# Kernel optimization log

Measured on AMD Instinct MI355X. Metric: run time of the kernel, lower is better.

## Reference

```python
import jax, jax.numpy as jnp
import numpy as np

B, N_X, N_A, DIM = 2, 2048, 2048, 1024
HEADS, DH = 16, 64
SEG = 256
ROPE_THETA = 10000.0


def mh_rmsnorm(t, gamma):
    # t: [b,h,n,d], gamma: [h,1,d]; F.normalize(dim=-1) * gamma * sqrt(d)
    norm = jnp.linalg.norm(t, axis=-1, keepdims=True)
    return t / jnp.clip(norm, 1e-12) * gamma * (DH ** 0.5)


def apply_rope(t):
    # t: [b,h,n,d]; GPT-NeoX style half-split rotary over packed positions
    n = t.shape[2]
    half = DH // 2
    inv_freq = ROPE_THETA ** (-jnp.arange(0, half, dtype=jnp.float32) / half)
    freqs = jnp.arange(n, dtype=jnp.float32)[:, None] * inv_freq[None, :]  # [n, half]
    cos, sin = jnp.cos(freqs), jnp.sin(freqs)
    t1, t2 = t[..., :half], t[..., half:]
    return jnp.concatenate([t1 * cos - t2 * sin, t2 * cos + t1 * sin], axis=-1)


def infini_attention(q, k, v, beta):
    # q,k,v: [b,h,n,d]; causal local attention per segment + recurrent linear memory
    b, h, n, d = q.shape
    s = n // SEG
    scale = d ** -0.5
    gate = jax.nn.sigmoid(beta).reshape(1, h, 1, 1)
    causal = jnp.tril(jnp.ones((SEG, SEG), dtype=bool))

    def to_segs(t):  # -> [s, b, h, SEG, d]
        return jnp.moveaxis(t.reshape(b, h, s, SEG, d), 2, 0)

    qs, ks, vs = to_segs(q), to_segs(k), to_segs(v)

    def step(carry, inp):
        M, z = carry  # M: [b,h,d,d], z: [b,h,d]
        q_s, k_s, v_s = inp
        sq = jax.nn.elu(q_s) + 1.0
        sk = jax.nn.elu(k_s) + 1.0
        # memory retrieval
        num = jnp.einsum('bhld,bhde->bhle', sq, M)
        den = jnp.einsum('bhld,bhd->bhl', sq, z)[..., None] + 1e-6
        a_mem = num / den
        # local causal attention within segment
        scores = jnp.einsum('bhid,bhjd->bhij', q_s, k_s) * scale
        scores = jnp.where(causal, scores, -jnp.inf)
        a_loc = jnp.einsum('bhij,bhjd->bhid', jax.nn.softmax(scores, axis=-1), v_s)
        out = gate * a_mem + (1.0 - gate) * a_loc
        # memory update
        M = M + jnp.einsum('bhld,bhle->bhde', sk, v_s)
        z = z + sk.sum(axis=2)
        return (M, z), out

    M0 = jnp.zeros((b, h, d, d), dtype=q.dtype)
    z0 = jnp.zeros((b, h, d), dtype=q.dtype)
    _, outs = jax.lax.scan(step, (M0, z0), (qs, ks, vs))  # [s,b,h,SEG,d]
    return jnp.moveaxis(outs, 0, 2).reshape(b, h, n, d)


def setup_inputs() -> dict:
    key = jax.random.key(0)
    ks = jax.random.split(key, 4)
    scale = DIM ** -0.5
    x = jax.random.normal(ks[0], (B, N_X, DIM), dtype=jnp.float32)
    a = jax.random.normal(ks[1], (B, N_A, DIM), dtype=jnp.float32)
    w_qkv_x = jax.random.normal(ks[2], (DIM, 3 * HEADS * DH), dtype=jnp.float32) * scale
    w_qkv_a = jax.random.normal(ks[3], (DIM, 3 * HEADS * DH), dtype=jnp.float32) * scale
    g = lambda: jnp.ones((HEADS, 1, DH), dtype=jnp.float32)
    beta = jnp.zeros((HEADS,), dtype=jnp.float32)
    return {"x": x, "a": a, "w_qkv_x": w_qkv_x, "w_qkv_a": w_qkv_a,
            "gq_x": g(), "gk_x": g(), "gq_a": g(), "gk_a": g(), "beta": beta}


def _split_heads(t):
    b, n, _ = t.shape
    q, k, v = jnp.split(t, 3, axis=-1)
    r = lambda u: u.reshape(b, n, HEADS, DH).transpose(0, 2, 1, 3)
    return r(q), r(k), r(v)


def reference(x, a, w_qkv_x, w_qkv_a, gq_x, gk_x, gq_a, gk_a, beta):
    q_x, k_x, v_x = _split_heads(x @ w_qkv_x)
    q_a, k_a, v_a = _split_heads(a @ w_qkv_a)
    q_x, k_x = mh_rmsnorm(q_x, gq_x), mh_rmsnorm(k_x, gk_x)
    q_a, k_a = mh_rmsnorm(q_a, gq_a), mh_rmsnorm(k_a, gk_a)
    # pack: a-stream first, then x-stream (matches pack([._a, ._x]))
    q = jnp.concatenate([q_a, q_x], axis=2)
    k = jnp.concatenate([k_a, k_x], axis=2)
    v = jnp.concatenate([v_a, v_x], axis=2)
    q, k = apply_rope(q), apply_rope(k)
    out = infini_attention(q, k, v, beta)  # [b,h,n_a+n_x,d]
    out_a, out_x = out[:, :, :N_A], out[:, :, N_A:]
    merge = lambda t: t.transpose(0, 2, 1, 3).reshape(t.shape[0], t.shape[2], HEADS * DH)
    return merge(out_x), merge(out_a)
```

## Files before the change

kernel.cpp:

```cpp
#include <hip/hip_runtime.h>

#define HEADS 16
#define DH    64
#define NA    2048
#define NX    2048
#define NTOT  4096
#define DIMK  1024
#define NQKV  3072
#define SEG   256
#define NSEG  16

typedef float          f32x4  __attribute__((ext_vector_type(4)));
typedef short          bf16x8 __attribute__((ext_vector_type(8)));
typedef unsigned int   u32x4  __attribute__((ext_vector_type(4)));

__device__ __forceinline__ unsigned short f2bf(float f){
  unsigned int u = __builtin_bit_cast(unsigned int, f);
  unsigned int r = 0x7fffu + ((u >> 16) & 1u);
  return (unsigned short)((u + r) >> 16);
}
__device__ __forceinline__ float bf2f(unsigned short u){
  return __builtin_bit_cast(float, ((unsigned int)u) << 16);
}

__global__ __launch_bounds__(256) void zero_kernel(float* __restrict__ out, int n){
  int i = blockIdx.x * 256 + threadIdx.x;
  if (i < n) out[i] = 0.f;
}

__global__ __launch_bounds__(256) void cvt_kernel(const float* __restrict__ src,
                                                  unsigned short* __restrict__ dst, int n4){
  int i = blockIdx.x * 256 + threadIdx.x;
  if (i >= n4) return;
  float4 v = ((const float4*)src)[i];
  ushort4 o;
  o.x = f2bf(v.x); o.y = f2bf(v.y); o.z = f2bf(v.z); o.w = f2bf(v.w);
  ((ushort4*)dst)[i] = o;
}

__global__ __launch_bounds__(256) void wtr_kernel(const float* __restrict__ W,
                                                  unsigned short* __restrict__ WT){
  __shared__ float tile[32][33];
  int c0 = blockIdx.x * 32, k0 = blockIdx.y * 32;
  int tx = threadIdx.x, ty = threadIdx.y;
  #pragma unroll
  for (int i = 0; i < 32; i += 8) tile[ty+i][tx] = W[(size_t)(k0+ty+i)*NQKV + c0 + tx];
  __syncthreads();
  #pragma unroll
  for (int i = 0; i < 32; i += 8) WT[(size_t)(c0+ty+i)*DIMK + k0 + tx] = f2bf(tile[tx][ty+i]);
}

__global__ __launch_bounds__(256) void rope_tab_kernel(float* __restrict__ tab){
  const int idx = blockIdx.x * 256 + threadIdx.x;
  const int n = idx >> 5, d = idx & 31;
  const float ang = (float)n * expf(-(float)d * 0.28782313662425572f);
  float sn, cs;
  sincosf(ang, &sn, &cs);
  float2 p; p.x = cs; p.y = sn;
  ((float2*)tab)[idx] = p;
}

__global__ __launch_bounds__(256,2) void gemm_qkv_kernel(
    const unsigned short* __restrict__ Xb, const unsigned short* __restrict__ Ab,
    const unsigned short* __restrict__ WTx, const unsigned short* __restrict__ WTa,
    unsigned short* __restrict__ qb, unsigned short* __restrict__ kb,
    unsigned short* __restrict__ vt,
    const float* __restrict__ gqx, const float* __restrict__ gkx,
    const float* __restrict__ gqa, const float* __restrict__ gka,
    const float* __restrict__ tab)
{
  __shared__ __align__(16) unsigned short As[128*32];
  __shared__ __align__(16) unsigned short Bs[128*32];
  const int strm = blockIdx.z;
  const unsigned short* Xp = strm ? Ab  : Xb;
  const unsigned short* Wp = strm ? WTa : WTx;
  const float* gq = strm ? gqa : gqx;
  const float* gk = strm ? gka : gkx;
  const int n_off = strm ? 0 : NA;

  const int tid  = threadIdx.x;
  const int lane = tid & 63, w = tid >> 6;
  const int wr = w >> 1, wc = w & 1;
  const int li = lane & 15, lg = lane >> 4;
  const int m0 = blockIdx.y * 128, c0 = blockIdx.x * 128;

  const int srow = lane >> 2;
  const int sslot = lane & 3;
  const int sswz = sslot ^ (srow & 3) ^ ((srow >> 2) & 3);
  const int rswz = (li & 3) ^ ((li >> 2) & 3);

  f32x4 acc[4][4] = {};

  for (int k0 = 0; k0 < DIMK; k0 += 32){
    __syncthreads();
    #pragma unroll
    for (int jj = 0; jj < 2; jj++){
      const int j = 2*w + jj;
      const int r = j*16 + srow;
      __builtin_amdgcn_global_load_lds(
        (const __attribute__((address_space(1))) unsigned int*)(Xp + (size_t)(m0+r)*DIMK + k0 + sswz*8),
        (__attribute__((address_space(3))) unsigned int*)(As + j*512), 16, 0, 0);
      __builtin_amdgcn_global_load_lds(
        (const __attribute__((address_space(1))) unsigned int*)(Wp + (size_t)(c0+r)*DIMK + k0 + sswz*8),
        (__attribute__((address_space(3))) unsigned int*)(Bs + j*512), 16, 0, 0);
    }
    __syncthreads();
    bf16x8 af[4], bf[4];
    const int slot = (lg ^ rswz) * 8;
    #pragma unroll
    for (int m = 0; m < 4; m++){
      const int r = wr*64 + m*16 + li;
      af[m] = *(const bf16x8*)(&As[r*32 + slot]);
    }
    #pragma unroll
    for (int n = 0; n < 4; n++){
      const int r = wc*64 + n*16 + li;
      bf[n] = *(const bf16x8*)(&Bs[r*32 + slot]);
    }
    #pragma unroll
    for (int m = 0; m < 4; m++)
      #pragma unroll
      for (int n = 0; n < 4; n++)
        acc[m][n] = __builtin_amdgcn_mfma_f32_16x16x32_bf16(af[m], bf[n], acc[m][n], 0, 0, 0);
  }

  const int colbase = c0 + wc*64;
  const int which = colbase >> 10;
  const int h = (colbase >> 6) & 15;

  if (which < 2){
    const float* gv = (which == 0) ? gq : gk;
    unsigned short* dstb = (which == 0) ? qb : kb;
    float gl[4];
    #pragma unroll
    for (int n = 0; n < 4; n++) gl[n] = gv[h*64 + n*16 + li];
    #pragma unroll
    for (int m = 0; m < 4; m++){
      #pragma unroll
      for (int r = 0; r < 4; r++){
        float ss = acc[m][0][r]*acc[m][0][r] + acc[m][1][r]*acc[m][1][r]
                 + acc[m][2][r]*acc[m][2][r] + acc[m][3][r]*acc[m][3][r];
        ss += __shfl_xor(ss, 1, 64);
        ss += __shfl_xor(ss, 2, 64);
        ss += __shfl_xor(ss, 4, 64);
        ss += __shfl_xor(ss, 8, 64);
        const float sc = 8.0f / fmaxf(sqrtf(ss), 1e-12f);
        float v0 = acc[m][0][r]*sc*gl[0], v1 = acc[m][1][r]*sc*gl[1];
        float v2 = acc[m][2][r]*sc*gl[2], v3 = acc[m][3][r]*sc*gl[3];
        const int row = m0 + wr*64 + m*16 + lg*4 + r;
        const int bb = row >> 11, nn = row & 2047;
        const int n_g = nn + n_off;
        const float2 cs0 = ((const float2*)tab)[n_g*32 + li];
        const float2 cs1 = ((const float2*)tab)[n_g*32 + 16 + li];
        const float o0 = v0*cs0.x - v2*cs0.y;
        const float o1 = v1*cs1.x - v3*cs1.y;
        const float o2 = v2*cs0.x + v0*cs0.y;
        const float o3 = v3*cs1.x + v1*cs1.y;
        unsigned short* drow = dstb + ((size_t)(bb*HEADS + h)*NTOT + (size_t)n_g)*64;
        drow[li]      = f2bf(o0);
        drow[16 + li] = f2bf(o1);
        drow[32 + li] = f2bf(o2);
        drow[48 + li] = f2bf(o3);
      }
    }
  } else {
    #pragma unroll
    for (int m = 0; m < 4; m++){
      #pragma unroll
      for (int r = 0; r < 4; r++){
        const int row = m0 + wr*64 + m*16 + lg*4 + r;
        const int bb = row >> 11, nn = row & 2047;
        const int n_g = nn + n_off;
        unsigned short* vbase = vt + (size_t)(bb*HEADS + h)*DH*NTOT + n_g;
        #pragma unroll
        for (int n = 0; n < 4; n++)
          vbase[(size_t)(n*16 + li)*NTOT] = f2bf(acc[m][n][r]);
      }
    }
  }
}

__global__ __launch_bounds__(256,2) void segG_kernel(const unsigned short* __restrict__ kb,
                                                     const unsigned short* __restrict__ vt,
                                                     float* __restrict__ G, float* __restrict__ zc){
  __shared__ unsigned short skT[64*264];
  __shared__ unsigned short Vts[64*264];
  const int blk = blockIdx.x;
  const int bh = blk >> 4, s = blk & 15;
  const int tid = threadIdx.x;
  const int w = tid >> 6, lane = tid & 63;
  const int li = lane & 15, lg = lane >> 4;
  const size_t segoffb = ((size_t)bh * NTOT + (size_t)s * SEG) * DH;

  #pragma unroll
  for (int it = 0; it < 8; it++){
    const int idx = tid + it*256;
    const int e = idx >> 5, jc = idx & 31;
    *(u32x4*)(Vts + e*264 + jc*8) =
      *(const u32x4*)(vt + (size_t)bh*DH*NTOT + (size_t)e*NTOT + s*SEG + jc*8);
  }
  #pragma unroll
  for (int it = 0; it < 8; it++){
    const int idx = tid + it*256;
    const int l = idx >> 3, dc = idx & 7;
    bf16x8 kk = *(const bf16x8*)(kb + segoffb + (size_t)l*64 + dc*8);
    #pragma unroll
    for (int t2 = 0; t2 < 8; t2++){
      const float xx = bf2f((unsigned short)kk[t2]);
      skT[(dc*8 + t2)*264 + l] = f2bf(xx > 0.f ? xx + 1.f : __expf(xx));
    }
  }
  __syncthreads();

  {
    const int d = tid >> 2, q = tid & 3;
    float zz = 0.f;
    #pragma unroll
    for (int u = 0; u < 8; u++){
      bf16x8 vv = *(const bf16x8*)(skT + d*264 + q*64 + u*8);
      #pragma unroll
      for (int t2 = 0; t2 < 8; t2++)
        zz += bf2f((unsigned short)vv[t2]);
    }
    zz += __shfl_xor(zz, 1, 64);
    zz += __shfl_xor(zz, 2, 64);
    if (q == 0) zc[(size_t)blk*64 + d] = zz;
  }

  f32x4 acc[4] = {};
  #pragma unroll
  for (int k0 = 0; k0 < 256; k0 += 32){
    bf16x8 af = *(const bf16x8*)(skT + (w*16 + li)*264 + k0 + lg*8);
    #pragma unroll
    for (int n = 0; n < 4; n++){
      bf16x8 bf = *(const bf16x8*)(Vts + (n*16 + li)*264 + k0 + lg*8);
      acc[n] = __builtin_amdgcn_mfma_f32_16x16x32_bf16(af, bf, acc[n], 0, 0, 0);
    }
  }
  float* Gout = G + (size_t)blk * DH * DH;
  #pragma unroll
  for (int n = 0; n < 4; n++)
    #pragma unroll
    for (int r = 0; r < 4; r++)
      Gout[(w*16 + lg*4 + r)*64 + n*16 + li] = acc[n][r];
}

__global__ __launch_bounds__(256) void prefix_kernel(const float* __restrict__ G,
                                                     const float* __restrict__ zc,
                                                     float* __restrict__ Mp, float* __restrict__ zp){
  const int bh = blockIdx.x, tid = threadIdx.x;
  float run[16];
  #pragma unroll
  for (int k = 0; k < 16; k++) run[k] = 0.f;
  for (int s = 0; s < NSEG; s++){
    const size_t base = ((size_t)bh * NSEG + s) * DH * DH;
    #pragma unroll
    for (int k = 0; k < 16; k++){
      Mp[base + tid + 256*k] = run[k];
      run[k] += G[base + tid + 256*k];
    }
  }
  if (tid < DH){
    float rz = 0.f;
    for (int s = 0; s < NSEG; s++){
      zp[((size_t)bh*NSEG + s)*DH + tid] = rz;
      rz += zc[((size_t)bh*NSEG + s)*DH + tid];
    }
  }
}

__global__ __launch_bounds__(256,1) void attn_mfma_kernel(
    const unsigned short* __restrict__ qb, const unsigned short* __restrict__ kb,
    const unsigned short* __restrict__ vt, const float* __restrict__ Mp,
    const float* __restrict__ zp, const float* __restrict__ beta,
    float* __restrict__ out)
{
  __shared__ unsigned short Qs[256*72];
  __shared__ unsigned short KSs[256*72];
  __shared__ unsigned short Vts[64*264];
  __shared__ unsigned short Ps[4*64*72];
  __shared__ unsigned short Mts[64*72];
  __shared__ float den_s[256];
  __shared__ float zsh[64];

  const int blk = blockIdx.x;
  const int s = blk & 15, bh = blk >> 4;
  const int h = bh & 15, b = bh >> 4;
  const int tid = threadIdx.x;
  const int w = tid >> 6, lane = tid & 63;
  const int li = lane & 15, lg = lane >> 4;
  const size_t segoffb = ((size_t)bh * NTOT + (size_t)s * SEG) * DH;

  #pragma unroll
  for (int it = 0; it < 8; it++){
    const int idx = tid + it*256;
    const int row = idx >> 3, jc = idx & 7;
    *(u32x4*)(Qs  + row*72 + jc*8) = *(const u32x4*)(qb + segoffb + (size_t)row*64 + jc*8);
    *(u32x4*)(KSs + row*72 + jc*8) = *(const u32x4*)(kb + segoffb + (size_t)row*64 + jc*8);
  }
  #pragma unroll
  for (int it = 0; it < 8; it++){
    const int idx = tid + it*256;
    const int e = idx >> 5, jc = idx & 31;
    *(u32x4*)(Vts + e*264 + jc*8) =
      *(const u32x4*)(vt + (size_t)bh*DH*NTOT + (size_t)e*NTOT + s*SEG + jc*8);
  }
  #pragma unroll
  for (int it = 0; it < 16; it++){
    const int idx = tid + it*256;
    const int d = idx >> 6, e = idx & 63;
    Mts[e*72 + d] = f2bf(Mp[(size_t)blk*4096 + d*64 + e]);
  }
  if (tid < 64) zsh[tid] = zp[(size_t)blk*64 + tid];
  __syncthreads();

  f32x4 o_acc[4][4] = {};
  float denr[4] = {0.f, 0.f, 0.f, 0.f};
  const int qrow0 = w*64;
  bf16x8 qf[4][2];
  #pragma unroll
  for (int it = 0; it < 4; it++)
    #pragma unroll
    for (int kb2 = 0; kb2 < 2; kb2++)
      qf[it][kb2] = *(const bf16x8*)(Qs + (qrow0 + it*16 + li)*72 + kb2*32 + lg*8);

  for (int c = 0; c <= w; c++){
    f32x4 st[4][4] = {};
    #pragma unroll
    for (int jt = 0; jt < 4; jt++){
      bf16x8 kf0 = *(const bf16x8*)(KSs + (c*64 + jt*16 + li)*72 + 0  + lg*8);
      bf16x8 kf1 = *(const bf16x8*)(KSs + (c*64 + jt*16 + li)*72 + 32 + lg*8);
      #pragma unroll
      for (int it = 0; it < 4; it++){
        st[jt][it] = __builtin_amdgcn_mfma_f32_16x16x32_bf16(kf0, qf[it][0], st[jt][it], 0, 0, 0);
        st[jt][it] = __builtin_amdgcn_mfma_f32_16x16x32_bf16(kf1, qf[it][1], st[jt][it], 0, 0, 0);
      }
    }
    const bool diag = (c == w);
    #pragma unroll
    for (int jt = 0; jt < 4; jt++){
      #pragma unroll
      for (int it = 0; it < 4; it++){
        f32x4 p = st[jt][it];
        unsigned pb[4];
        #pragma unroll
        for (int r = 0; r < 4; r++){
          float pe = __expf(p[r] * 0.125f);
          if (diag && (jt*16 + lg*4 + r > it*16 + li)) pe = 0.f;
          pb[r] = __builtin_bit_cast(unsigned, pe) & 0xFFFF0000u;
          p[r] = __builtin_bit_cast(float, pb[r]);
        }
        denr[it] += (p[0] + p[1]) + (p[2] + p[3]);
        uint2 pkk;
        pkk.x = (pb[0] >> 16) | pb[1];
        pkk.y = (pb[2] >> 16) | pb[3];
        *(uint2*)(Ps + w*4608 + (it*16 + li)*72 + jt*16 + lg*4) = pkk;
      }
    }
    bf16x8 pf[4][2];
    #pragma unroll
    for (int it = 0; it < 4; it++)
      #pragma unroll
      for (int kb2 = 0; kb2 < 2; kb2++)
        pf[it][kb2] = *(const bf16x8*)(Ps + w*4608 + (it*16 + li)*72 + kb2*32 + lg*8);
    #pragma unroll
    for (int et = 0; et < 4; et++){
      bf16x8 vf0 = *(const bf16x8*)(Vts + (et*16 + li)*264 + c*64 + 0  + lg*8);
      bf16x8 vf1 = *(const bf16x8*)(Vts + (et*16 + li)*264 + c*64 + 32 + lg*8);
      #pragma unroll
      for (int it = 0; it < 4; it++){
        o_acc[it][et] = __builtin_amdgcn_mfma_f32_16x16x32_bf16(pf[it][0], vf0, o_acc[it][et], 0, 0, 0);
        o_acc[it][et] = __builtin_amdgcn_mfma_f32_16x16x32_bf16(pf[it][1], vf1, o_acc[it][et], 0, 0, 0);
      }
    }
  }

  #pragma unroll
  for (int it = 0; it < 4; it++){
    denr[it] += __shfl_xor(denr[it], 16, 64);
    denr[it] += __shfl_xor(denr[it], 32, 64);
  }
  if (lane < 16){
    #pragma unroll
    for (int it = 0; it < 4; it++) den_s[qrow0 + it*16 + lane] = denr[it];
  }
  const float gate = 1.f / (1.f + __expf(-beta[h]));
  __syncthreads();

  {
    const int i = tid;
    float sqv[64];
    float denm = 0.f;
    #pragma unroll
    for (int u = 0; u < 8; u++){
      bf16x8 qv = *(const bf16x8*)(Qs + i*72 + u*8);
      #pragma unroll
      for (int t2 = 0; t2 < 8; t2++){
        float x = bf2f((unsigned short)qv[t2]);
        float sq = x > 0.f ? x + 1.f : __expf(x);
        sqv[u*8 + t2] = sq;
        denm += sq * zsh[u*8 + t2];
      }
    }
    const float c2 = gate / (denm + 1e-6f);
    #pragma unroll
    for (int u = 0; u < 16; u++){
      uint2 pw;
      pw.x = f2bf(sqv[u*4]*c2)   | ((unsigned)f2bf(sqv[u*4+1]*c2) << 16);
      pw.y = f2bf(sqv[u*4+2]*c2) | ((unsigned)f2bf(sqv[u*4+3]*c2) << 16);
      *(uint2*)(KSs + i*72 + u*4) = pw;
    }
  }
  __syncthreads();

  #pragma unroll
  for (int it = 0; it < 4; it++){
    #pragma unroll
    for (int r = 0; r < 4; r++){
      const float c1 = (1.f - gate) / den_s[qrow0 + it*16 + lg*4 + r];
      #pragma unroll
      for (int et = 0; et < 4; et++) o_acc[it][et][r] *= c1;
    }
  }
  #pragma unroll
  for (int kb2 = 0; kb2 < 2; kb2++){
    bf16x8 mf[4];
    #pragma unroll
    for (int et = 0; et < 4; et++)
      mf[et] = *(const bf16x8*)(Mts + (et*16 + li)*72 + kb2*32 + lg*8);
    #pragma unroll
    for (int it = 0; it < 4; it++){
      bf16x8 sf = *(const bf16x8*)(KSs + (qrow0 + it*16 + li)*72 + kb2*32 + lg*8);
      #pragma unroll
      for (int et = 0; et < 4; et++)
        o_acc[it][et] = __builtin_amdgcn_mfma_f32_16x16x32_bf16(sf, mf[et], o_acc[it][et], 0, 0, 0);
    }
  }

  #pragma unroll
  for (int it = 0; it < 4; it++){
    #pragma unroll
    for (int r = 0; r < 4; r++){
      const int n_g = s*SEG + qrow0 + it*16 + lg*4 + r;
      size_t o;
      if (n_g >= NA) o = ((size_t)b * NX + (size_t)(n_g - NA)) * 1024 + h * 64;
      else           o = 4194304u + ((size_t)b * NA + (size_t)n_g) * 1024 + h * 64;
      #pragma unroll
      for (int et = 0; et < 4; et++)
        out[o + et*16 + li] = o_acc[it][et][r];
    }
  }
}

extern "C" void kernel_launch(void* const* d_in, const int* in_sizes, int n_in,
                              void* d_out, int out_size, void* d_ws, size_t ws_size,
                              hipStream_t stream)
{
  (void)ws_size;
  const int expect[9] = {4194304, 4194304, 3145728, 3145728, 1024, 1024, 1024, 1024, 16};
  bool ok = (n_in == 9);
  if (ok) for (int i = 0; i < 9; i++) if (in_sizes[i] != expect[i]) { ok = false; break; }
  float* out = (float*)d_out;
  if (!ok){
    zero_kernel<<<dim3((out_size + 255)/256), dim3(256), 0, stream>>>(out, out_size);
    return;
  }

  const float* x    = (const float*)d_in[0];
  const float* a    = (const float*)d_in[1];
  const float* wx   = (const float*)d_in[2];
  const float* wa   = (const float*)d_in[3];
  const float* gqx  = (const float*)d_in[4];
  const float* gkx  = (const float*)d_in[5];
  const float* gqa  = (const float*)d_in[6];
  const float* gka  = (const float*)d_in[7];
  const float* beta = (const float*)d_in[8];

  char* wsb = (char*)d_ws;
  unsigned short* qb  = (unsigned short*)wsb;
  unsigned short* kb  = qb + 8388608;
  unsigned short* vtb = kb + 8388608;
  unsigned short* Xb  = vtb + 8388608;
  unsigned short* Ab  = Xb + 4194304;
  unsigned short* WTx = Ab + 4194304;
  unsigned short* WTa = WTx + 3145728;
  float* ropetab = (float*)(WTa + 3145728);
  float* G   = ropetab + 262144;
  float* Mp  = G + 2097152;
  float* zc  = Mp + 2097152;
  float* zpb = zc + 32768;

  cvt_kernel<<<dim3(4096), dim3(256), 0, stream>>>(x, Xb, 1048576);
  cvt_kernel<<<dim3(4096), dim3(256), 0, stream>>>(a, Ab, 1048576);
  wtr_kernel<<<dim3(96,32), dim3(32,8), 0, stream>>>(wx, WTx);
  wtr_kernel<<<dim3(96,32), dim3(32,8), 0, stream>>>(wa, WTa);
  rope_tab_kernel<<<dim3(512), dim3(256), 0, stream>>>(ropetab);
  gemm_qkv_kernel<<<dim3(24,32,2), dim3(256), 0, stream>>>(Xb, Ab, WTx, WTa, qb, kb, vtb,
                                                           gqx, gkx, gqa, gka, ropetab);
  segG_kernel<<<dim3(512), dim3(256), 0, stream>>>(kb, vtb, G, zc);
  prefix_kernel<<<dim3(32), dim3(256), 0, stream>>>(G, zc, Mp, zpb);
  attn_mfma_kernel<<<dim3(512), dim3(256), 0, stream>>>(qb, kb, vtb, Mp, zpb, beta, out);
}
```

Measured before the change: 156.4 us.

## Double-buffer QKV GEMM LDS tiles and remap blocks across XCDs

The QKV projection GEMM now uses two LDS buffers, so the global-to-LDS load for the next k-slice is issued before the MFMA work on the current slice. This halves the barriers per k-step and hides load latency. The launch also changes from a 3D grid to a flat 1D grid, with a block-ID remap that groups consecutive logical tiles onto the same XCD (bid&7) for better L2 reuse. LDS use doubles to 32KB per block, which could limit occupancy under launch_bounds(256,2). There is also a hazard risk: a buffer is restaged right after one barrier while other waves may still be reading it.

```diff
diff --git a/kernel.cpp b/kernel.cpp
--- a/kernel.cpp
+++ b/kernel.cpp
@@ -69,9 +69,18 @@
     const float* __restrict__ gqa, const float* __restrict__ gka,
     const float* __restrict__ tab)
 {
-  __shared__ __align__(16) unsigned short As[128*32];
-  __shared__ __align__(16) unsigned short Bs[128*32];
-  const int strm = blockIdx.z;
+  __shared__ __align__(16) unsigned short As0[128*32];
+  __shared__ __align__(16) unsigned short Bs0[128*32];
+  __shared__ __align__(16) unsigned short As1[128*32];
+  __shared__ __align__(16) unsigned short Bs1[128*32];
+
+  const int bid = blockIdx.x;
+  const int lid = (bid & 7) * 192 + (bid >> 3);
+  const int strm = lid / 768;
+  const int rem  = lid - strm * 768;
+  const int c0 = (rem >> 5) * 128;
+  const int m0 = (rem & 31) * 128;
+
   const unsigned short* Xp = strm ? Ab  : Xb;
   const unsigned short* Wp = strm ? WTa : WTx;
   const float* gq = strm ? gqa : gqx;
@@ -82,7 +91,6 @@
   const int lane = tid & 63, w = tid >> 6;
   const int wr = w >> 1, wc = w & 1;
   const int li = lane & 15, lg = lane >> 4;
-  const int m0 = blockIdx.y * 128, c0 = blockIdx.x * 128;
 
   const int srow = lane >> 2;
   const int sslot = lane & 3;
@@ -91,37 +99,44 @@
 
   f32x4 acc[4][4] = {};
 
-  for (int k0 = 0; k0 < DIMK; k0 += 32){
-    __syncthreads();
+  auto stage = [&](unsigned short* AsX, unsigned short* BsX, int kk){
     #pragma unroll
     for (int jj = 0; jj < 2; jj++){
       const int j = 2*w + jj;
       const int r = j*16 + srow;
       __builtin_amdgcn_global_load_lds(
-        (const __attribute__((address_space(1))) unsigned int*)(Xp + (size_t)(m0+r)*DIMK + k0 + sswz*8),
-        (__attribute__((address_space(3))) unsigned int*)(As + j*512), 16, 0, 0);
+        (const __attribute__((address_space(1))) unsigned int*)(Xp + (size_t)(m0+r)*DIMK + kk + sswz*8),
+        (__attribute__((address_space(3))) unsigned int*)(AsX + j*512), 16, 0, 0);
       __builtin_amdgcn_global_load_lds(
-        (const __attribute__((address_space(1))) unsigned int*)(Wp + (size_t)(c0+r)*DIMK + k0 + sswz*8),
-        (__attribute__((address_space(3))) unsigned int*)(Bs + j*512), 16, 0, 0);
-    }
-    __syncthreads();
+        (const __attribute__((address_space(1))) unsigned int*)(Wp + (size_t)(c0+r)*DIMK + kk + sswz*8),
+        (__attribute__((address_space(3))) unsigned int*)(BsX + j*512), 16, 0, 0);
+    }
+  };
+  auto compute = [&](const unsigned short* AsX, const unsigned short* BsX){
     bf16x8 af[4], bf[4];
     const int slot = (lg ^ rswz) * 8;
     #pragma unroll
-    for (int m = 0; m < 4; m++){
-      const int r = wr*64 + m*16 + li;
-      af[m] = *(const bf16x8*)(&As[r*32 + slot]);
-    }
-    #pragma unroll
-    for (int n = 0; n < 4; n++){
-      const int r = wc*64 + n*16 + li;
-      bf[n] = *(const bf16x8*)(&Bs[r*32 + slot]);
-    }
+    for (int m = 0; m < 4; m++)
+      af[m] = *(const bf16x8*)(&AsX[(wr*64 + m*16 + li)*32 + slot]);
+    #pragma unroll
+    for (int n = 0; n < 4; n++)
+      bf[n] = *(const bf16x8*)(&BsX[(wc*64 + n*16 + li)*32 + slot]);
     #pragma unroll
     for (int m = 0; m < 4; m++)
       #pragma unroll
       for (int n = 0; n < 4; n++)
         acc[m][n] = __builtin_amdgcn_mfma_f32_16x16x32_bf16(af[m], bf[n], acc[m][n], 0, 0, 0);
+  };
+
+  stage(As0, Bs0, 0);
+  __syncthreads();
+  for (int t = 0; t < 32; t += 2){
+    stage(As1, Bs1, (t+1)*32);
+    compute(As0, Bs0);
+    __syncthreads();
+    if (t + 2 < 32) stage(As0, Bs0, (t+2)*32);
+    compute(As1, Bs1);
+    __syncthreads();
   }
 
   const int colbase = c0 + wc*64;
@@ -495,8 +510,8 @@
   wtr_kernel<<<dim3(96,32), dim3(32,8), 0, stream>>>(wx, WTx);
   wtr_kernel<<<dim3(96,32), dim3(32,8), 0, stream>>>(wa, WTa);
   rope_tab_kernel<<<dim3(512), dim3(256), 0, stream>>>(ropetab);
-  gemm_qkv_kernel<<<dim3(24,32,2), dim3(256), 0, stream>>>(Xb, Ab, WTx, WTa, qb, kb, vtb,
-                                                           gqx, gkx, gqa, gka, ropetab);
+  gemm_qkv_kernel<<<dim3(1536), dim3(256), 0, stream>>>(Xb, Ab, WTx, WTa, qb, kb, vtb,
+                                                        gqx, gkx, gqa, gka, ropetab);
   segG_kernel<<<dim3(512), dim3(256), 0, stream>>>(kb, vtb, G, zc);
   prefix_kernel<<<dim3(32), dim3(256), 0, stream>>>(G, zc, Mp, zpb);
   attn_mfma_kernel<<<dim3(512), dim3(256), 0, stream>>>(qb, kb, vtb, Mp, zpb, beta, out);
```

Result: faster. 150.7 us (-3.6%).
